# Kernel optimization log

Measured on AMD Instinct MI355X. Metric: run time of the kernel, lower is better.

Reference implementation:

```python
import jax, jax.numpy as jnp
import numpy as np

# Dims: B=32 batch, C=64 feat channels, Np=192 priors, No=72 row offsets,
# Ns=36 pooled sample points (maxpool kernel 2), Hd=64 fc hidden.
B, C, Np, No, Hd = 32, 64, 192, 72, 64
NS_POOL = 2  # n_offsets // sample_points
REG_DIM = No + 4  # reg_layers output


def bilinear_sample(feat, gx, gy):
    """torch F.grid_sample(align_corners=True) equivalent for in-range coords.
    feat: [B,C,H,W]; gx,gy: [B,Np,S] normalized to [-1,1]. -> [B,C,Np,S]."""
    Bb, Cc, H, W = feat.shape
    ix = (gx + 1.0) * 0.5 * (W - 1)
    iy = (gy + 1.0) * 0.5 * (H - 1)
    ix0f = jnp.floor(ix); iy0f = jnp.floor(iy)
    wx = ix - ix0f; wy = iy - iy0f
    ix0 = jnp.clip(ix0f.astype(jnp.int32), 0, W - 1)
    iy0 = jnp.clip(iy0f.astype(jnp.int32), 0, H - 1)
    ix1 = jnp.clip(ix0 + 1, 0, W - 1)
    iy1 = jnp.clip(iy0 + 1, 0, H - 1)
    ff = feat.reshape(Bb, Cc, H * W)
    S = gx.shape[1] * gx.shape[2]
    def gather(iy_, ix_):
        idx = (iy_ * W + ix_).reshape(Bb, 1, S)
        g = jnp.take_along_axis(ff, jnp.broadcast_to(idx, (Bb, Cc, S)), axis=2)
        return g.reshape(Bb, Cc, gx.shape[1], gx.shape[2])
    v00 = gather(iy0, ix0); v01 = gather(iy0, ix1)
    v10 = gather(iy1, ix0); v11 = gather(iy1, ix1)
    wx = wx[:, None]; wy = wy[:, None]  # broadcast over C
    return (v00 * (1 - wx) * (1 - wy) + v01 * wx * (1 - wy)
            + v10 * (1 - wx) * wy + v11 * wx * wy)


def _mlp2(h, Ws, bs):
    # two stacked Linear+ReLU layers (num_fc=2)
    for i in range(2):
        h = jax.nn.relu(h @ Ws[i] + bs[i])
    return h


def setup_inputs() -> dict:
    key = jax.random.key(0)
    ks = jax.random.split(key, 24)
    w = lambda k, sh: jax.random.normal(k, sh, dtype=jnp.float32) * 0.05
    return {
        "x0": jax.random.normal(ks[0], (B, C, 40, 100), dtype=jnp.float32),
        "x1": jax.random.normal(ks[1], (B, C, 20, 50), dtype=jnp.float32),
        "x2": jax.random.normal(ks[2], (B, C, 10, 25), dtype=jnp.float32),
        "prior_xs0": jax.random.uniform(ks[3], (Np, No), dtype=jnp.float32),
        "l_weight": w(ks[4], (No,)),              # self.l embedding, sigmoid gate
        "lsgi_w": w(ks[5], (3, C, C)),            # per-stage lsgi projection
        "fc_w": w(ks[6], (C, Hd)), "fc_b": w(ks[7], (Hd,)),
        "cls_w": w(ks[8], (2, Hd, Hd)), "cls_b": w(ks[9], (2, Hd)),
        "cls_ow": w(ks[10], (Hd, 2)), "cls_ob": w(ks[11], (2,)),
        "reg_w": w(ks[12], (2, Hd, Hd)), "reg_b": w(ks[13], (2, Hd)),
        "reg_ow": w(ks[14], (Hd, REG_DIM)), "reg_ob": w(ks[15], (REG_DIM,)),
        "loc_w": w(ks[16], (2, Hd, Hd)), "loc_b": w(ks[17], (2, Hd)),
        "loc_ow": w(ks[18], (Hd, 1)), "loc_ob": w(ks[19], (1,)),
    }


def reference(x0, x1, x2, prior_xs0, l_weight, lsgi_w, fc_w, fc_b,
              cls_w, cls_b, cls_ow, cls_ob, reg_w, reg_b, reg_ow, reg_ob,
              loc_w, loc_b, loc_ow, loc_ob):
    pyramid = [x2, x1, x0]  # reversed: coarsest level first (stage 0)
    prior_feat_ys = jnp.linspace(1.0, 0.0, No, dtype=jnp.float32)
    gy = jnp.broadcast_to((prior_feat_ys * 2.0 - 1.0)[None, None, :], (B, Np, No))
    prior_xs = jnp.broadcast_to(prior_xs0[None], (B, Np, No))
    gate = jax.nn.sigmoid(l_weight)[:, None]  # [No,1]
    stage_feats = []
    outs = []
    for s in range(3):
        gx = prior_xs * 2.0 - 1.0
        pooled = bilinear_sample(pyramid[s], gx, gy)          # [B,C,Np,No]
        pooled = jnp.transpose(pooled, (0, 2, 3, 1)) * gate   # [B,Np,No,C]
        pooled = jax.nn.relu(jnp.einsum('bnoc,cd->bnod', pooled, lsgi_w[s]))
        # MaxPool2d kernel (2,1) over the offset axis -> Ns=36 sample points
        comp = pooled.reshape(B, Np, No // NS_POOL, NS_POOL, C).max(axis=3)
        stage_feats.append(comp)
        # cross-stage fusion (global head): mean over stages and sample points
        fused = jnp.stack(stage_feats, 0).mean(axis=0).mean(axis=2)  # [B,Np,C]
        fc = jax.nn.relu(fused @ fc_w + fc_b)                        # [B,Np,Hd]
        cls = _mlp2(fc, cls_w, cls_b) @ cls_ow + cls_ob              # [B,Np,2]
        reg = _mlp2(fc, reg_w, reg_b) @ reg_ow + reg_ob              # [B,Np,No+4]
        loc = _mlp2(fc, loc_w, loc_b) @ loc_ow + loc_ob              # [B,Np,1]
        outs.append(jnp.concatenate([cls, reg, loc], axis=-1))      # [B,Np,79]
        # refine anchors for next stage from predicted xs
        prior_xs = jax.nn.sigmoid(reg[..., 4:])
    return jnp.stack(outs, axis=0)  # [3,B,Np,79]
```

## Files before the change

kernel.cpp:

```cpp
#include <hip/hip_runtime.h>
#include <hip/hip_bf16.h>

#define Bq   32
#define Cq   64
#define NPq  192
#define NOq  72
#define PTS  (NPq * NOq)
#define REGD 76
#define OUTD 79

typedef __attribute__((ext_vector_type(8))) short short8;
typedef __attribute__((ext_vector_type(4))) float float4v;

__device__ inline unsigned short f2bf(float x) {
    __hip_bfloat16 h = __float2bfloat16(x);
    return *reinterpret_cast<unsigned short*>(&h);
}
__device__ inline float bf2f(unsigned short u) {
    unsigned int x = ((unsigned int)u) << 16;
    float f;
    __builtin_memcpy(&f, &x, 4);
    return f;
}

__global__ __launch_bounds__(256) void build_tables_kernel(
    const float* __restrict__ f0,
    const float* __restrict__ f1,
    const float* __restrict__ f2,
    const float* __restrict__ lw,
    unsigned short* __restrict__ t0,
    unsigned short* __restrict__ t1,
    unsigned short* __restrict__ t2)
{
    __shared__ float sRow[64 * 101];

    const int tid = threadIdx.x;
    const int o   = blockIdx.x / 96;
    const int sb  = blockIdx.x - o * 96;
    const int s   = sb >> 5;
    const int b   = sb & 31;

    const float* feat; unsigned short* tab; int H, W;
    if (s == 0)      { feat = f0; tab = t0; H = 10; W = 25; }
    else if (s == 1) { feat = f1; tab = t1; H = 20; W = 50; }
    else             { feat = f2; tab = t2; H = 40; W = 100; }
    const int Wp = W + 1;

    const float ys = 1.0f - (float)o * (1.0f / 71.0f);
    const float iy = ys * (float)(H - 1);
    const float fy = floorf(iy);
    const float wy = iy - fy;
    int iy0 = (int)fy; iy0 = iy0 < 0 ? 0 : (iy0 > H - 1 ? H - 1 : iy0);
    const int iy1 = (iy0 + 1 > H - 1) ? H - 1 : iy0 + 1;
    const float gate = 1.0f / (1.0f + __expf(-lw[o]));

    const float* fb = feat + (size_t)b * 64 * H * W;
    const int iy0W = iy0 * W, iy1W = iy1 * W;

    const int tot = 64 * W;
    for (int idx = tid; idx < tot; idx += 256) {
        const int c = idx / W;
        const int x = idx - c * W;
        const float* f = fb + c * (H * W);
        sRow[c * Wp + x] = ((1.0f - wy) * f[iy0W + x] + wy * f[iy1W + x]) * gate;
    }
    __syncthreads();

    unsigned short* to = tab + (size_t)(b * NOq + o) * Wp * 64;
    const int tot2 = Wp * 64;
    for (int idx = tid; idx < tot2; idx += 256) {
        const int x = idx >> 6;
        const int c = idx & 63;
        const int xx = (x < W) ? x : (W - 1);
        to[idx] = f2bf(sRow[c * Wp + xx]);
    }
}

template<int W>
__global__ __launch_bounds__(256) void fused_pool_head_kernel(
    const unsigned short* __restrict__ tab,
    const float* __restrict__ xsrc, const int xstride,
    const float* __restrict__ lsgi,
    float* __restrict__ sumFeat,
    const int stage,
    const float* __restrict__ fc_w,  const float* __restrict__ fc_b,
    const float* __restrict__ cls_w, const float* __restrict__ cls_b,
    const float* __restrict__ cls_ow, const float* __restrict__ cls_ob,
    const float* __restrict__ reg_w, const float* __restrict__ reg_b,
    const float* __restrict__ reg_ow, const float* __restrict__ reg_ob,
    const float* __restrict__ loc_w, const float* __restrict__ loc_b,
    const float* __restrict__ loc_ow, const float* __restrict__ loc_ob,
    float* __restrict__ out, float* __restrict__ xs_next)
{
    constexpr int Wp = W + 1;
    __shared__ __align__(16) float sF [8][68];
    __shared__ __align__(16) float sC [8][68];
    __shared__ __align__(16) float sT1[8][68];
    __shared__ __align__(16) float sT2[8][68];
    __shared__ __align__(16) float sWt[4864];

    const int tid  = threadIdx.x;
    const int w    = tid >> 6;
    const int lane = tid & 63;
    const int ng   = blockIdx.x >> 5;
    const int b    = blockIdx.x & 31;
    const int npair = ng * 4 + w;

    short8 wf[4][2];
    {
        const int kb = ((lane >> 4) & 3) * 8;
        const int dl = lane & 15;
        #pragma unroll
        for (int ks = 0; ks < 2; ++ks)
            #pragma unroll
            for (int dt = 0; dt < 4; ++dt) {
                union { unsigned short u[8]; short8 v; } pk;
                #pragma unroll
                for (int j = 0; j < 8; ++j)
                    pk.u[j] = f2bf(lsgi[(ks * 32 + kb + j) * 64 + dt * 16 + dl]);
                wf[dt][ks] = pk.v;
            }
    }

    const unsigned short* tb = tab + (size_t)b * NOq * Wp * 64;
    const float* xp = xsrc + (size_t)xstride * b;
    const int m  = lane & 15;
    const int kg = lane >> 4;
    const int nt0 = npair * 9;

    float sums0[4] = {0.f, 0.f, 0.f, 0.f};
    float sums1[4] = {0.f, 0.f, 0.f, 0.f};

    #pragma unroll
    for (int ntl = 0; ntl < 9; ++ntl) {
        const int pt = (nt0 + ntl) * 16 + m;
        const int o  = pt % NOq;
        float ixf = xp[pt] * (float)(W - 1);
        ixf = fminf(fmaxf(ixf, 0.0f), (float)(W - 1));
        const float fx = floorf(ixf);
        const float wx = ixf - fx;
        const int ix0 = (int)fx;

        const unsigned short* col = tb + ((size_t)o * Wp + ix0) * 64 + kg * 8;
        const short8 a00 = *(const short8*)(col);
        const short8 a01 = *(const short8*)(col + 64);
        const short8 a10 = *(const short8*)(col + 32);
        const short8 a11 = *(const short8*)(col + 96);

        float wxr[4];
        #pragma unroll
        for (int j = 0; j < 4; ++j) wxr[j] = __shfl(wx, kg * 4 + j);

        const bool hi = (ntl * 16 + (kg * 4)) >= NOq;
        #pragma unroll
        for (int dt = 0; dt < 4; ++dt) {
            float4v c0 = {0.f, 0.f, 0.f, 0.f};
            float4v c1 = {0.f, 0.f, 0.f, 0.f};
            c0 = __builtin_amdgcn_mfma_f32_16x16x32_bf16(a00, wf[dt][0], c0, 0, 0, 0);
            c0 = __builtin_amdgcn_mfma_f32_16x16x32_bf16(a10, wf[dt][1], c0, 0, 0, 0);
            c1 = __builtin_amdgcn_mfma_f32_16x16x32_bf16(a01, wf[dt][0], c1, 0, 0, 0);
            c1 = __builtin_amdgcn_mfma_f32_16x16x32_bf16(a11, wf[dt][1], c1, 0, 0, 0);
            const float v0 = c0[0] + wxr[0] * (c1[0] - c0[0]);
            const float v1 = c0[1] + wxr[1] * (c1[1] - c0[1]);
            const float v2 = c0[2] + wxr[2] * (c1[2] - c0[2]);
            const float v3 = c0[3] + wxr[3] * (c1[3] - c0[3]);
            const float pm0 = fmaxf(fmaxf(v0, v1), 0.f);
            const float pm1 = fmaxf(fmaxf(v2, v3), 0.f);
            const float add = pm0 + pm1;
            if (hi) sums1[dt] += add; else sums0[dt] += add;
        }
    }

    #pragma unroll
    for (int dt = 0; dt < 4; ++dt) {
        float v0 = sums0[dt], v1 = sums1[dt];
        v0 += __shfl_xor(v0, 16); v0 += __shfl_xor(v0, 32);
        v1 += __shfl_xor(v1, 16); v1 += __shfl_xor(v1, 32);
        sums0[dt] = v0; sums1[dt] = v1;
    }

    const float invS = 1.0f / (float)(stage + 1);
    if (lane < 16) {
        const size_t row0 = (size_t)(b * NPq + npair * 2) * 64;
        #pragma unroll
        for (int dt = 0; dt < 4; ++dt) {
            const int d = dt * 16 + lane;
            float t0 = sums0[dt] * (1.0f / 36.0f);
            float t1 = sums1[dt] * (1.0f / 36.0f);
            float* p0 = sumFeat + row0 + d;
            float* p1 = sumFeat + row0 + 64 + d;
            if (stage > 0) { t0 += *p0; t1 += *p1; }
            *p0 = t0; *p1 = t1;
            sF[2 * w][d]     = t0 * invS;
            sF[2 * w + 1][d] = t1 * invS;
        }
    }

    const int pt2 = tid >> 5;
    const int dh  = tid & 31;
    const int d0  = dh * 2;
    const int p0g = b * NPq + ng * 8;

    auto gemm64 = [&](const float (*src)[68], float (*dst)[68],
                      const float* __restrict__ gw, const float* __restrict__ gb) {
        __syncthreads();
        #pragma unroll
        for (int i = 0; i < 4; ++i)
            *(float4*)&sWt[(i * 256 + tid) * 4] = *(const float4*)&gw[(i * 256 + tid) * 4];
        __syncthreads();
        float a0 = gb[d0], a1 = gb[d0 + 1];
        #pragma unroll 8
        for (int k = 0; k < 64; ++k) {
            const float av = src[pt2][k];
            const float2 w2 = *(const float2*)&sWt[k * 64 + d0];
            a0 += av * w2.x; a1 += av * w2.y;
        }
        dst[pt2][d0]     = fmaxf(a0, 0.f);
        dst[pt2][d0 + 1] = fmaxf(a1, 0.f);
    };

    gemm64(sF, sC, fc_w, fc_b);

    gemm64(sC,  sT1, cls_w,        cls_b);
    gemm64(sT1, sT2, cls_w + 4096, cls_b + 64);
    __syncthreads();
    if (tid < 16) {
        const int p = tid >> 1, d = tid & 1;
        float z = cls_ob[d];
        #pragma unroll 8
        for (int k = 0; k < 64; ++k) z += sT2[p][k] * cls_ow[k * 2 + d];
        out[(size_t)(p0g + p) * OUTD + d] = z;
    }

    gemm64(sC,  sT1, reg_w,        reg_b);
    gemm64(sT1, sT2, reg_w + 4096, reg_b + 64);
    __syncthreads();
    for (int idx = tid; idx < 64 * REGD; idx += 256) sWt[idx] = reg_ow[idx];
    __syncthreads();
    {
        float* orow = out + (size_t)(p0g + pt2) * OUTD;
        float* xsp  = xs_next + (size_t)(p0g + pt2) * NOq;
        for (int j = dh; j < REGD; j += 32) {
            float z = reg_ob[j];
            #pragma unroll 8
            for (int k = 0; k < 64; ++k) z += sT2[pt2][k] * sWt[k * REGD + j];
            orow[2 + j] = z;
            if (j >= 4) xsp[j - 4] = 1.0f / (1.0f + __expf(-z));
        }
    }

    gemm64(sC,  sT1, loc_w,        loc_b);
    gemm64(sT1, sT2, loc_w + 4096, loc_b + 64);
    __syncthreads();
    if (tid < 8) {
        float z = loc_ob[0];
        #pragma unroll 8
        for (int k = 0; k < 64; ++k) z += sT2[tid][k] * loc_ow[k];
        out[(size_t)(p0g + tid) * OUTD + 78] = z;
    }
}

extern "C" void kernel_launch(void* const* d_in, const int* in_sizes, int n_in,
                              void* d_out, int out_size, void* d_ws, size_t ws_size,
                              hipStream_t stream)
{
    const float* x0        = (const float*)d_in[0];
    const float* x1        = (const float*)d_in[1];
    const float* x2        = (const float*)d_in[2];
    const float* prior_xs0 = (const float*)d_in[3];
    const float* l_weight  = (const float*)d_in[4];
    const float* lsgi_w    = (const float*)d_in[5];
    const float* fc_w      = (const float*)d_in[6];
    const float* fc_b      = (const float*)d_in[7];
    const float* cls_w     = (const float*)d_in[8];
    const float* cls_b     = (const float*)d_in[9];
    const float* cls_ow    = (const float*)d_in[10];
    const float* cls_ob    = (const float*)d_in[11];
    const float* reg_w     = (const float*)d_in[12];
    const float* reg_b     = (const float*)d_in[13];
    const float* reg_ow    = (const float*)d_in[14];
    const float* reg_ob    = (const float*)d_in[15];
    const float* loc_w     = (const float*)d_in[16];
    const float* loc_b     = (const float*)d_in[17];
    const float* loc_ow    = (const float*)d_in[18];
    const float* loc_ob    = (const float*)d_in[19];

    float* out     = (float*)d_out;
    float* sumFeat = (float*)d_ws;
    float* xs      = sumFeat + (size_t)Bq * NPq * Cq;
    unsigned short* tab0 = (unsigned short*)(xs + (size_t)Bq * PTS);
    unsigned short* tab1 = tab0 + (size_t)Bq * NOq * 26  * 64;
    unsigned short* tab2 = tab1 + (size_t)Bq * NOq * 51  * 64;

    hipLaunchKernelGGL(build_tables_kernel, dim3(3 * Bq * NOq), dim3(256), 0, stream,
                       x2, x1, x0, l_weight, tab0, tab1, tab2);

    for (int s = 0; s < 3; ++s) {
        const float* xsrc = (s == 0) ? prior_xs0 : xs;
        const int xstr    = (s == 0) ? 0 : PTS;
        const unsigned short* tb = (s == 0) ? tab0 : (s == 1) ? tab1 : tab2;
        float* outS = out + (size_t)s * Bq * NPq * OUTD;
        if (s == 0)
            hipLaunchKernelGGL((fused_pool_head_kernel<25>), dim3(Bq * 24), dim3(256), 0, stream,
                               tb, xsrc, xstr, lsgi_w + s * 4096, sumFeat, s,
                               fc_w, fc_b, cls_w, cls_b, cls_ow, cls_ob,
                               reg_w, reg_b, reg_ow, reg_ob,
                               loc_w, loc_b, loc_ow, loc_ob, outS, xs);
        else if (s == 1)
            hipLaunchKernelGGL((fused_pool_head_kernel<50>), dim3(Bq * 24), dim3(256), 0, stream,
                               tb, xsrc, xstr, lsgi_w + s * 4096, sumFeat, s,
                               fc_w, fc_b, cls_w, cls_b, cls_ow, cls_ob,
                               reg_w, reg_b, reg_ow, reg_ob,
                               loc_w, loc_b, loc_ow, loc_ob, outS, xs);
        else
            hipLaunchKernelGGL((fused_pool_head_kernel<100>), dim3(Bq * 24), dim3(256), 0, stream,
                               tb, xsrc, xstr, lsgi_w + s * 4096, sumFeat, s,
                               fc_w, fc_b, cls_w, cls_b, cls_ow, cls_ob,
                               reg_w, reg_b, reg_ow, reg_ob,
                               loc_w, loc_b, loc_ow, loc_ob, outS, xs);
    }
}
```

Before: 249.7 us.

## Double-buffer head weights in LDS and prefetch next gather tile

The head MLP chain now uses two shared weight buffers. Each GEMM stage loads the next stage's weights into registers while it computes, then stores them to the other buffer, which removes one barrier and a serialized global load per stage. The bilinear gather loop precomputes column pointers and prefetches the next tile's four bf16 vectors ahead of the MFMAs. The table build kernel is templated on H and W so sizes are compile-time constants. The cost is higher register and LDS use per block, which can lower occupancy.

```diff
diff --git a/kernel.cpp b/kernel.cpp
--- a/kernel.cpp
+++ b/kernel.cpp
@@ -21,6 +21,44 @@
     float f;
     __builtin_memcpy(&f, &x, 4);
     return f;
+}
+
+template<int H, int W>
+__device__ __forceinline__ void build_one(
+    const float* __restrict__ feat, unsigned short* __restrict__ tab,
+    const float* __restrict__ lw, const int b, const int o,
+    float* __restrict__ sRow, const int tid)
+{
+    constexpr int Wp = W + 1;
+
+    const float ys = 1.0f - (float)o * (1.0f / 71.0f);
+    const float iy = ys * (float)(H - 1);
+    const float fy = floorf(iy);
+    const float wy = iy - fy;
+    int iy0 = (int)fy; iy0 = iy0 < 0 ? 0 : (iy0 > H - 1 ? H - 1 : iy0);
+    const int iy1 = (iy0 + 1 > H - 1) ? H - 1 : iy0 + 1;
+    const float gate = 1.0f / (1.0f + __expf(-lw[o]));
+
+    const float* fb = feat + (size_t)b * 64 * H * W;
+    const int iy0W = iy0 * W, iy1W = iy1 * W;
+
+    constexpr int tot = 64 * W;
+    for (int idx = tid; idx < tot; idx += 256) {
+        const int c = idx / W;
+        const int x = idx - c * W;
+        const float* f = fb + c * (H * W);
+        sRow[c * Wp + x] = ((1.0f - wy) * f[iy0W + x] + wy * f[iy1W + x]) * gate;
+    }
+    __syncthreads();
+
+    unsigned short* to = tab + (size_t)(b * NOq + o) * Wp * 64;
+    constexpr int tot2 = Wp * 64;
+    for (int idx = tid; idx < tot2; idx += 256) {
+        const int x = idx >> 6;
+        const int c = idx & 63;
+        const int xx = (x < W) ? x : (W - 1);
+        to[idx] = f2bf(sRow[c * Wp + xx]);
+    }
 }
 
 __global__ __launch_bounds__(256) void build_tables_kernel(
@@ -33,47 +71,15 @@
     unsigned short* __restrict__ t2)
 {
     __shared__ float sRow[64 * 101];
-
     const int tid = threadIdx.x;
     const int o   = blockIdx.x / 96;
     const int sb  = blockIdx.x - o * 96;
     const int s   = sb >> 5;
     const int b   = sb & 31;
 
-    const float* feat; unsigned short* tab; int H, W;
-    if (s == 0)      { feat = f0; tab = t0; H = 10; W = 25; }
-    else if (s == 1) { feat = f1; tab = t1; H = 20; W = 50; }
-    else             { feat = f2; tab = t2; H = 40; W = 100; }
-    const int Wp = W + 1;
-
-    const float ys = 1.0f - (float)o * (1.0f / 71.0f);
-    const float iy = ys * (float)(H - 1);
-    const float fy = floorf(iy);
-    const float wy = iy - fy;
-    int iy0 = (int)fy; iy0 = iy0 < 0 ? 0 : (iy0 > H - 1 ? H - 1 : iy0);
-    const int iy1 = (iy0 + 1 > H - 1) ? H - 1 : iy0 + 1;
-    const float gate = 1.0f / (1.0f + __expf(-lw[o]));
-
-    const float* fb = feat + (size_t)b * 64 * H * W;
-    const int iy0W = iy0 * W, iy1W = iy1 * W;
-
-    const int tot = 64 * W;
-    for (int idx = tid; idx < tot; idx += 256) {
-        const int c = idx / W;
-        const int x = idx - c * W;
-        const float* f = fb + c * (H * W);
-        sRow[c * Wp + x] = ((1.0f - wy) * f[iy0W + x] + wy * f[iy1W + x]) * gate;
-    }
-    __syncthreads();
-
-    unsigned short* to = tab + (size_t)(b * NOq + o) * Wp * 64;
-    const int tot2 = Wp * 64;
-    for (int idx = tid; idx < tot2; idx += 256) {
-        const int x = idx >> 6;
-        const int c = idx & 63;
-        const int xx = (x < W) ? x : (W - 1);
-        to[idx] = f2bf(sRow[c * Wp + xx]);
-    }
+    if (s == 0)      build_one<10, 25 >(f0, t0, lw, b, o, sRow, tid);
+    else if (s == 1) build_one<20, 50 >(f1, t1, lw, b, o, sRow, tid);
+    else             build_one<40, 100>(f2, t2, lw, b, o, sRow, tid);
 }
 
 template<int W>
@@ -97,7 +103,8 @@
     __shared__ __align__(16) float sC [8][68];
     __shared__ __align__(16) float sT1[8][68];
     __shared__ __align__(16) float sT2[8][68];
-    __shared__ __align__(16) float sWt[4864];
+    __shared__ __align__(16) float sWtA[4864];
+    __shared__ __align__(16) float sWtB[4864];
 
     const int tid  = threadIdx.x;
     const int w    = tid >> 6;
@@ -105,6 +112,10 @@
     const int ng   = blockIdx.x >> 5;
     const int b    = blockIdx.x & 31;
     const int npair = ng * 4 + w;
+
+    #pragma unroll
+    for (int i = 0; i < 4; ++i)
+        *(float4*)&sWtA[(i * 256 + tid) * 4] = *(const float4*)&fc_w[(i * 256 + tid) * 4];
 
     short8 wf[4][2];
     {
@@ -128,38 +139,51 @@
     const int kg = lane >> 4;
     const int nt0 = npair * 9;
 
-    float sums0[4] = {0.f, 0.f, 0.f, 0.f};
-    float sums1[4] = {0.f, 0.f, 0.f, 0.f};
-
+    float wxa[9];
+    const unsigned short* cola[9];
     #pragma unroll
-    for (int ntl = 0; ntl < 9; ++ntl) {
-        const int pt = (nt0 + ntl) * 16 + m;
+    for (int t = 0; t < 9; ++t) {
+        const int pt = (nt0 + t) * 16 + m;
         const int o  = pt % NOq;
         float ixf = xp[pt] * (float)(W - 1);
         ixf = fminf(fmaxf(ixf, 0.0f), (float)(W - 1));
         const float fx = floorf(ixf);
-        const float wx = ixf - fx;
-        const int ix0 = (int)fx;
-
-        const unsigned short* col = tb + ((size_t)o * Wp + ix0) * 64 + kg * 8;
-        const short8 a00 = *(const short8*)(col);
-        const short8 a01 = *(const short8*)(col + 64);
-        const short8 a10 = *(const short8*)(col + 32);
-        const short8 a11 = *(const short8*)(col + 96);
+        wxa[t] = ixf - fx;
+        cola[t] = tb + ((size_t)o * Wp + (int)fx) * 64 + kg * 8;
+    }
+
+    float sums0[4] = {0.f, 0.f, 0.f, 0.f};
+    float sums1[4] = {0.f, 0.f, 0.f, 0.f};
+
+    short8 cur0, cur1, cur2, cur3;
+    cur0 = *(const short8*)(cola[0]);
+    cur1 = *(const short8*)(cola[0] + 64);
+    cur2 = *(const short8*)(cola[0] + 32);
+    cur3 = *(const short8*)(cola[0] + 96);
+
+    #pragma unroll
+    for (int ntl = 0; ntl < 9; ++ntl) {
+        short8 nx0, nx1, nx2, nx3;
+        if (ntl < 8) {
+            nx0 = *(const short8*)(cola[ntl + 1]);
+            nx1 = *(const short8*)(cola[ntl + 1] + 64);
+            nx2 = *(const short8*)(cola[ntl + 1] + 32);
+            nx3 = *(const short8*)(cola[ntl + 1] + 96);
+        }
 
         float wxr[4];
         #pragma unroll
-        for (int j = 0; j < 4; ++j) wxr[j] = __shfl(wx, kg * 4 + j);
+        for (int j = 0; j < 4; ++j) wxr[j] = __shfl(wxa[ntl], kg * 4 + j);
 
         const bool hi = (ntl * 16 + (kg * 4)) >= NOq;
         #pragma unroll
         for (int dt = 0; dt < 4; ++dt) {
             float4v c0 = {0.f, 0.f, 0.f, 0.f};
             float4v c1 = {0.f, 0.f, 0.f, 0.f};
-            c0 = __builtin_amdgcn_mfma_f32_16x16x32_bf16(a00, wf[dt][0], c0, 0, 0, 0);
-            c0 = __builtin_amdgcn_mfma_f32_16x16x32_bf16(a10, wf[dt][1], c0, 0, 0, 0);
-            c1 = __builtin_amdgcn_mfma_f32_16x16x32_bf16(a01, wf[dt][0], c1, 0, 0, 0);
-            c1 = __builtin_amdgcn_mfma_f32_16x16x32_bf16(a11, wf[dt][1], c1, 0, 0, 0);
+            c0 = __builtin_amdgcn_mfma_f32_16x16x32_bf16(cur0, wf[dt][0], c0, 0, 0, 0);
+            c0 = __builtin_amdgcn_mfma_f32_16x16x32_bf16(cur2, wf[dt][1], c0, 0, 0, 0);
+            c1 = __builtin_amdgcn_mfma_f32_16x16x32_bf16(cur1, wf[dt][0], c1, 0, 0, 0);
+            c1 = __builtin_amdgcn_mfma_f32_16x16x32_bf16(cur3, wf[dt][1], c1, 0, 0, 0);
             const float v0 = c0[0] + wxr[0] * (c1[0] - c0[0]);
             const float v1 = c0[1] + wxr[1] * (c1[1] - c0[1]);
             const float v2 = c0[2] + wxr[2] * (c1[2] - c0[2]);
@@ -169,6 +193,7 @@
             const float add = pm0 + pm1;
             if (hi) sums1[dt] += add; else sums0[dt] += add;
         }
+        cur0 = nx0; cur1 = nx1; cur2 = nx2; cur3 = nx3;
     }
 
     #pragma unroll
@@ -201,28 +226,36 @@
     const int d0  = dh * 2;
     const int p0g = b * NPq + ng * 8;
 
-    auto gemm64 = [&](const float (*src)[68], float (*dst)[68],
-                      const float* __restrict__ gw, const float* __restrict__ gb) {
+    auto do_gemm = [&](const float (*src)[68], float (*dst)[68],
+                       const float* wbuf, const float* __restrict__ gb,
+                       const float* __restrict__ nextw, int nextn, float* nextbuf) {
         __syncthreads();
-        #pragma unroll
-        for (int i = 0; i < 4; ++i)
-            *(float4*)&sWt[(i * 256 + tid) * 4] = *(const float4*)&gw[(i * 256 + tid) * 4];
-        __syncthreads();
+        float4 pf[5];
+        const int n4 = nextn >> 2;
+        #pragma unroll
+        for (int i = 0; i < 5; ++i) {
+            const int idx = i * 256 + tid;
+            if (idx < n4) pf[i] = *(const float4*)&nextw[idx * 4];
+        }
         float a0 = gb[d0], a1 = gb[d0 + 1];
         #pragma unroll 8
         for (int k = 0; k < 64; ++k) {
             const float av = src[pt2][k];
-            const float2 w2 = *(const float2*)&sWt[k * 64 + d0];
+            const float2 w2 = *(const float2*)&wbuf[k * 64 + d0];
             a0 += av * w2.x; a1 += av * w2.y;
         }
         dst[pt2][d0]     = fmaxf(a0, 0.f);
         dst[pt2][d0 + 1] = fmaxf(a1, 0.f);
+        #pragma unroll
+        for (int i = 0; i < 5; ++i) {
+            const int idx = i * 256 + tid;
+            if (idx < n4) *(float4*)&nextbuf[idx * 4] = pf[i];
+        }
     };
 
-    gemm64(sF, sC, fc_w, fc_b);
-
-    gemm64(sC,  sT1, cls_w,        cls_b);
-    gemm64(sT1, sT2, cls_w + 4096, cls_b + 64);
+    do_gemm(sF,  sC,  sWtA, fc_b,       cls_w,        4096, sWtB);
+    do_gemm(sC,  sT1, sWtB, cls_b,      cls_w + 4096, 4096, sWtA);
+    do_gemm(sT1, sT2, sWtA, cls_b + 64, reg_w,        4096, sWtB);
     __syncthreads();
     if (tid < 16) {
         const int p = tid >> 1, d = tid & 1;
@@ -232,25 +265,31 @@
         out[(size_t)(p0g + p) * OUTD + d] = z;
     }
 
-    gemm64(sC,  sT1, reg_w,        reg_b);
-    gemm64(sT1, sT2, reg_w + 4096, reg_b + 64);
-    __syncthreads();
-    for (int idx = tid; idx < 64 * REGD; idx += 256) sWt[idx] = reg_ow[idx];
+    do_gemm(sC,  sT1, sWtB, reg_b,      reg_w + 4096, 4096,      sWtA);
+    do_gemm(sT1, sT2, sWtA, reg_b + 64, reg_ow,       64 * REGD, sWtB);
     __syncthreads();
     {
+        float4 pf[4];
+        #pragma unroll
+        for (int i = 0; i < 4; ++i)
+            pf[i] = *(const float4*)&loc_w[(i * 256 + tid) * 4];
+
         float* orow = out + (size_t)(p0g + pt2) * OUTD;
         float* xsp  = xs_next + (size_t)(p0g + pt2) * NOq;
         for (int j = dh; j < REGD; j += 32) {
             float z = reg_ob[j];
             #pragma unroll 8
-            for (int k = 0; k < 64; ++k) z += sT2[pt2][k] * sWt[k * REGD + j];
+            for (int k = 0; k < 64; ++k) z += sT2[pt2][k] * sWtB[k * REGD + j];
             orow[2 + j] = z;
             if (j >= 4) xsp[j - 4] = 1.0f / (1.0f + __expf(-z));
         }
-    }
-
-    gemm64(sC,  sT1, loc_w,        loc_b);
-    gemm64(sT1, sT2, loc_w + 4096, loc_b + 64);
+        #pragma unroll
+        for (int i = 0; i < 4; ++i)
+            *(float4*)&sWtA[(i * 256 + tid) * 4] = pf[i];
+    }
+
+    do_gemm(sC,  sT1, sWtA, loc_b,      loc_w + 4096, 4096, sWtB);
+    do_gemm(sT1, sT2, sWtB, loc_b + 64, loc_w,        0,    sWtA);
     __syncthreads();
     if (tid < 8) {
         float z = loc_ob[0];
```

After: 287.5 us. 1.15x slower.
